# Performance work log

Measured on AMD Instinct MI355X. Metric: run time of the kernel, lower is better.

## Reference

```python
import jax, jax.numpy as jnp
import numpy as np

MARGIN = 0.3

def _cdist(x):
    # pairwise euclidean distances, safe sqrt (zero grad at 0)
    sq = jnp.sum(x * x, axis=1)
    d2 = sq[:, None] + sq[None, :] - 2.0 * (x @ x.T)
    d2 = jnp.maximum(d2, 0.0)
    safe = jnp.where(d2 > 0, d2, 1.0)
    return jnp.where(d2 > 0, jnp.sqrt(safe), 0.0)

def setup_inputs() -> dict:
    key = jax.random.key(0)
    k1, k2 = jax.random.split(key)
    embeddings = jax.random.normal(k1, (4096, 128), dtype=jnp.float32)
    labels = jax.random.randint(k2, (4096,), 0, 256)
    return {"embeddings": embeddings, "labels": labels}

def reference(embeddings, labels):
    B = embeddings.shape[0]
    dist = _cdist(embeddings)                      # [B, B]
    same = labels[:, None] == labels[None, :]      # [B, B]
    eye = jnp.eye(B, dtype=bool)
    pos_mask = same & ~eye
    neg_mask = ~same
    neg_inf = jnp.array(-jnp.inf, dist.dtype)
    pos_inf = jnp.array(jnp.inf, dist.dtype)
    hard_pos = jnp.max(jnp.where(pos_mask, dist, neg_inf), axis=1)  # [B]
    hard_neg = jnp.min(jnp.where(neg_mask, dist, pos_inf), axis=1)  # [B]
    valid = jnp.any(pos_mask, axis=1) & jnp.any(neg_mask, axis=1)
    per_row = jax.nn.relu(hard_pos - hard_neg + MARGIN)
    per_row = jnp.where(valid, per_row, 0.0)
    num_valid = jnp.sum(valid.astype(dist.dtype))
    return jnp.sum(per_row) / jnp.maximum(num_valid, 1.0)
```

## Files before the change

kernel.cpp:

```cpp
#include <hip/hip_runtime.h>
#include <hip/hip_bf16.h>


typedef __attribute__((ext_vector_type(8))) short short8;
typedef __attribute__((ext_vector_type(4))) float f32x4;

#define MARGIN_F 0.3f
#define NEG_BIG -3.4e38f
#define POS_BIG 3.4e38f
#define WAITVM(N) __builtin_amdgcn_s_waitcnt(((N)&15)|((((N)>>4)&3)<<14)|(7<<4)|(15<<8))

__device__ __forceinline__ void gl_lds16(const void* g, void* l) {
    __builtin_amdgcn_global_load_lds(
        (const __attribute__((address_space(1))) void*)g,
        (__attribute__((address_space(3))) void*)l, 16, 0, 0);
}

__device__ inline unsigned short f2bf(float x) {
    union { __hip_bfloat16 h; unsigned short u; } c;
    c.h = __float2bfloat16(x);
    return c.u;
}

__global__ __launch_bounds__(256) void tl_prep(const float* __restrict__ E,
                                               unsigned short* __restrict__ Ebf,
                                               float* __restrict__ sqn,
                                               unsigned* __restrict__ accum) {
    int t = blockIdx.x * 256 + threadIdx.x;
    if (t < 4) accum[t] = 0u;
    int row = t >> 5;
    int kq = (t & 31) * 4;
    float4 v = *(const float4*)&E[(size_t)row * 128 + kq];
    float s = fmaf(v.x, v.x, fmaf(v.y, v.y, fmaf(v.z, v.z, v.w * v.w)));
    ushort4 h4;
    h4.x = f2bf(v.x); h4.y = f2bf(v.y); h4.z = f2bf(v.z); h4.w = f2bf(v.w);
    *(ushort4*)&Ebf[(size_t)row * 128 + kq] = h4;
#pragma unroll
    for (int m = 1; m < 32; m <<= 1) s += __shfl_xor(s, m);
    if ((t & 31) == 0) sqn[row] = s;
}

__global__ __launch_bounds__(256, 2) void tl_phase1(const unsigned short* __restrict__ Ebf,
                                                    const int* __restrict__ labels,
                                                    const float* __restrict__ sqn,
                                                    float* __restrict__ pmp,
                                                    float* __restrict__ pmn) {
    union SM {
        struct { unsigned short A[2][128 * 64]; unsigned short B[2][128 * 64]; } s;
        struct { float mp[128][32]; float mn[128][32];
                 float mpc[128][8]; float mnc[128][8]; } f;
    };
    __shared__ __align__(16) SM sm;

    const int tid = threadIdx.x;
    const int l = tid & 63, w = tid >> 6;
    const int wr = w >> 1, wc = w & 1;
    const int q = l >> 4, r16 = l & 15;

    int t = (int)blockIdx.x;
    int bx = (int)((65.0f - sqrtf((float)(4225 - 8 * t))) * 0.5f);
    while (bx * (65 - bx) / 2 > t) --bx;
    while ((bx + 1) * (64 - bx) / 2 <= t) ++bx;
    const int by = bx + (t - bx * (65 - bx) / 2);
    const int i0 = bx * 128, j0 = by * 128;
    const bool diagblk = (bx == by);

    const unsigned short* gA[4];
    const unsigned short* gB[4];
#pragma unroll
    for (int t2 = 0; t2 < 4; ++t2) {
        int s = w * 256 + t2 * 64 + l;
        int row = s >> 3, ch = (s & 7) ^ (row & 7);
        gA[t2] = Ebf + (size_t)(i0 + row) * 128 + ch * 8;
        gB[t2] = Ebf + (size_t)(j0 + row) * 128 + ch * 8;
    }

    int li[4][4], lj[4];
    float si[4][4], sj[4];
#pragma unroll
    for (int ti = 0; ti < 4; ++ti)
#pragma unroll
        for (int p = 0; p < 4; ++p) {
            int ci = i0 + wr * 64 + ti * 16 + q * 4 + p;
            li[ti][p] = labels[ci];
            si[ti][p] = sqn[ci];
        }
#pragma unroll
    for (int tj = 0; tj < 4; ++tj) {
        int cj = j0 + wc * 64 + tj * 16 + r16;
        lj[tj] = labels[cj];
        sj[tj] = sqn[cj];
    }

#pragma unroll
    for (int t2 = 0; t2 < 4; ++t2) {
        gl_lds16(gA[t2], &sm.s.A[0][w * 2048 + t2 * 512]);
        gl_lds16(gB[t2], &sm.s.B[0][w * 2048 + t2 * 512]);
    }
#pragma unroll
    for (int t2 = 0; t2 < 4; ++t2) {
        gl_lds16(gA[t2] + 64, &sm.s.A[1][w * 2048 + t2 * 512]);
        gl_lds16(gB[t2] + 64, &sm.s.B[1][w * 2048 + t2 * 512]);
    }

    f32x4 acc[4][4];
#pragma unroll
    for (int ti = 0; ti < 4; ++ti)
#pragma unroll
        for (int tj = 0; tj < 4; ++tj) acc[ti][tj] = (f32x4)0.0f;

#pragma unroll
    for (int kc = 0; kc < 2; ++kc) {
        if (kc == 0) WAITVM(8); else WAITVM(0);
        __builtin_amdgcn_s_barrier();
#pragma unroll
        for (int s = 0; s < 2; ++s) {
            short8 af[4], bf[4];
            const int cA = ((s * 4 + q) ^ (r16 & 7)) * 8;
#pragma unroll
            for (int t2 = 0; t2 < 4; ++t2) {
                af[t2] = *(const short8*)&sm.s.A[kc][(wr * 64 + t2 * 16 + r16) * 64 + cA];
                bf[t2] = *(const short8*)&sm.s.B[kc][(wc * 64 + t2 * 16 + r16) * 64 + cA];
            }
#pragma unroll
            for (int ti = 0; ti < 4; ++ti)
#pragma unroll
                for (int tj = 0; tj < 4; ++tj)
                    acc[ti][tj] = __builtin_amdgcn_mfma_f32_16x16x32_bf16(
                        af[ti], bf[tj], acc[ti][tj], 0, 0, 0);
        }
    }

    float mp[4][4], mn[4][4], mpc[4], mnc[4];
#pragma unroll
    for (int ti = 0; ti < 4; ++ti)
#pragma unroll
        for (int p = 0; p < 4; ++p) { mp[ti][p] = NEG_BIG; mn[ti][p] = POS_BIG; }
#pragma unroll
    for (int tj = 0; tj < 4; ++tj) {
        float cp = NEG_BIG, cn = POS_BIG;
#pragma unroll
        for (int ti = 0; ti < 4; ++ti)
#pragma unroll
            for (int p = 0; p < 4; ++p) {
                float g = acc[ti][tj][p];
                float vr = fmaf(-2.0f, g, sj[tj]);
                float vc = fmaf(-2.0f, g, si[ti][p]);
                bool same = (li[ti][p] == lj[tj]);
                bool self = diagblk &&
                    ((wr * 64 + ti * 16 + q * 4 + p) == (wc * 64 + tj * 16 + r16));
                mp[ti][p] = fmaxf(mp[ti][p], (same && !self) ? vr : NEG_BIG);
                mn[ti][p] = fminf(mn[ti][p], same ? POS_BIG : vr);
                cp = fmaxf(cp, (same && !self) ? vc : NEG_BIG);
                cn = fminf(cn, same ? POS_BIG : vc);
            }
        mpc[tj] = cp;
        mnc[tj] = cn;
    }

    __syncthreads();
#pragma unroll
    for (int ti = 0; ti < 4; ++ti)
#pragma unroll
        for (int p = 0; p < 4; ++p) {
            int rloc = wr * 64 + ti * 16 + q * 4 + p;
            sm.f.mp[rloc][wc * 16 + r16] = mp[ti][p];
            sm.f.mn[rloc][wc * 16 + r16] = mn[ti][p];
        }
#pragma unroll
    for (int tj = 0; tj < 4; ++tj) {
        int cloc = wc * 64 + tj * 16 + r16;
        sm.f.mpc[cloc][wr * 4 + q] = mpc[tj];
        sm.f.mnc[cloc][wr * 4 + q] = mnc[tj];
    }
    __syncthreads();
    {
        int row = tid >> 1, hf = tid & 1;
        const float4* P = (const float4*)&sm.f.mp[row][hf * 16];
        const float4* N = (const float4*)&sm.f.mn[row][hf * 16];
        float4 p0 = P[0], p1 = P[1], p2 = P[2], p3 = P[3];
        float4 n0 = N[0], n1 = N[1], n2 = N[2], n3 = N[3];
        float M = fmaxf(fmaxf(fmaxf(p0.x, p0.y), fmaxf(p0.z, p0.w)),
                        fmaxf(fmaxf(p1.x, p1.y), fmaxf(p1.z, p1.w)));
        M = fmaxf(M, fmaxf(fmaxf(fmaxf(p2.x, p2.y), fmaxf(p2.z, p2.w)),
                           fmaxf(fmaxf(p3.x, p3.y), fmaxf(p3.z, p3.w))));
        float m_ = fminf(fminf(fminf(n0.x, n0.y), fminf(n0.z, n0.w)),
                         fminf(fminf(n1.x, n1.y), fminf(n1.z, n1.w)));
        m_ = fminf(m_, fminf(fminf(fminf(n2.x, n2.y), fminf(n2.z, n2.w)),
                             fminf(fminf(n3.x, n3.y), fminf(n3.z, n3.w))));
        M = fmaxf(M, __shfl_xor(M, 1));
        m_ = fminf(m_, __shfl_xor(m_, 1));
        if (hf == 0) {
            pmp[(size_t)by * 4096 + i0 + row] = M;
            pmn[(size_t)by * 4096 + i0 + row] = m_;
        }
    }
    if (!diagblk && tid < 128) {
        const float4* P = (const float4*)&sm.f.mpc[tid][0];
        const float4* N = (const float4*)&sm.f.mnc[tid][0];
        float4 p0 = P[0], p1 = P[1];
        float4 n0 = N[0], n1 = N[1];
        float M = fmaxf(fmaxf(fmaxf(p0.x, p0.y), fmaxf(p0.z, p0.w)),
                        fmaxf(fmaxf(p1.x, p1.y), fmaxf(p1.z, p1.w)));
        float m_ = fminf(fminf(fminf(n0.x, n0.y), fminf(n0.z, n0.w)),
                         fminf(fminf(n1.x, n1.y), fminf(n1.z, n1.w)));
        pmp[(size_t)bx * 4096 + j0 + tid] = M;
        pmn[(size_t)bx * 4096 + j0 + tid] = m_;
    }
}

__global__ __launch_bounds__(256) void tl_phase2(const int* __restrict__ labels,
                                                 const float* __restrict__ pmp,
                                                 const float* __restrict__ pmn,
                                                 const float* __restrict__ sqn,
                                                 float* __restrict__ accum,
                                                 float* __restrict__ out) {
    __shared__ unsigned hist[256];
    __shared__ float sp[4], sv[4];
    int tid = threadIdx.x;
    hist[tid] = 0u;
    __syncthreads();
#pragma unroll
    for (int k = 0; k < 16; ++k) atomicAdd(&hist[labels[k * 256 + tid]], 1u);
    __syncthreads();

    int r = blockIdx.x * 256 + tid;
    float mp = NEG_BIG, mn = POS_BIG;
#pragma unroll
    for (int k = 0; k < 32; ++k) {
        mp = fmaxf(mp, pmp[(size_t)k * 4096 + r]);
        mn = fminf(mn, pmn[(size_t)k * 4096 + r]);
    }
    float si = sqn[r];
    unsigned cnt = hist[labels[r]];
    bool valid = (cnt >= 2u) && (cnt < 4096u);
    float hp = sqrtf(fmaxf(si + mp, 0.0f));
    float hn = sqrtf(fmaxf(si + mn, 0.0f));
    float pr = fmaxf(hp - hn + MARGIN_F, 0.0f);
    float s = valid ? pr : 0.0f;
    float n = valid ? 1.0f : 0.0f;
#pragma unroll
    for (int m = 1; m < 64; m <<= 1) {
        s += __shfl_xor(s, m);
        n += __shfl_xor(n, m);
    }
    if ((tid & 63) == 0) { sp[tid >> 6] = s; sv[tid >> 6] = n; }
    __syncthreads();
    if (tid == 0) {
        float ts = sp[0] + sp[1] + sp[2] + sp[3];
        float tn = sv[0] + sv[1] + sv[2] + sv[3];
        atomicAdd(&accum[0], ts);
        atomicAdd(&accum[1], tn);
        __threadfence();
        unsigned tk = atomicAdd((unsigned*)&accum[2], 1u);
        if (tk == 15u) {
            float a = atomicAdd(&accum[0], 0.0f);
            float b = atomicAdd(&accum[1], 0.0f);
            out[0] = a / fmaxf(b, 1.0f);
        }
    }
}

extern "C" void kernel_launch(void* const* d_in, const int* in_sizes, int n_in,
                              void* d_out, int out_size, void* d_ws, size_t ws_size,
                              hipStream_t stream) {
    const float* E = (const float*)d_in[0];
    const int* labels = (const int*)d_in[1];
    float* out = (float*)d_out;

    char* base = (char*)d_ws;
    unsigned short* Ebf = (unsigned short*)base;
    float* pmp = (float*)(base + (1u << 20));
    float* pmn = (float*)(base + (1u << 20) + (512u << 10));
    float* sqn = (float*)(base + (2u << 20));
    float* accum = (float*)(base + (2u << 20) + (16u << 10));

    tl_prep<<<512, 256, 0, stream>>>(E, Ebf, sqn, (unsigned*)accum);
    tl_phase1<<<528, 256, 0, stream>>>(Ebf, labels, sqn, pmp, pmn);
    tl_phase2<<<16, 256, 0, stream>>>(labels, pmp, pmn, sqn, accum, out);
}
```

Measured before the change: 72.20 us.

## Fuse final reduction into main kernel via atomic min/max and last-block finish

Replaces the per-block-column partial max/min arrays and the separate phase2 kernel with global atomicMax/atomicMin on order-preserving unsigned encodings of the floats. A completion counter lets the last block compute the label histogram, the hinge terms and the final mean, which removes one kernel launch and the 32-way partial reduction pass. In exchange there are atomic contention on 4096 addresses, a single block doing the whole final pass serially, and added fences.

```diff
diff --git a/kernel.cpp b/kernel.cpp
--- a/kernel.cpp
+++ b/kernel.cpp
@@ -22,12 +22,24 @@
     return c.u;
 }
 
+__device__ __forceinline__ unsigned encf(float x) {
+    unsigned u = __float_as_uint(x);
+    return (u >> 31) ? ~u : (u | 0x80000000u);
+}
+__device__ __forceinline__ float decf(unsigned k) {
+    return (k & 0x80000000u) ? __uint_as_float(k ^ 0x80000000u)
+                             : __uint_as_float(~k);
+}
+
 __global__ __launch_bounds__(256) void tl_prep(const float* __restrict__ E,
                                                unsigned short* __restrict__ Ebf,
                                                float* __restrict__ sqn,
-                                               unsigned* __restrict__ accum) {
+                                               unsigned* __restrict__ mpg,
+                                               unsigned* __restrict__ mng,
+                                               unsigned* __restrict__ cnt) {
     int t = blockIdx.x * 256 + threadIdx.x;
-    if (t < 4) accum[t] = 0u;
+    if (t < 4096) { mpg[t] = 0u; mng[t] = 0xFFFFFFFFu; }
+    if (t == 0) cnt[0] = 0u;
     int row = t >> 5;
     int kq = (t & 31) * 4;
     float4 v = *(const float4*)&E[(size_t)row * 128 + kq];
@@ -40,17 +52,22 @@
     if ((t & 31) == 0) sqn[row] = s;
 }
 
-__global__ __launch_bounds__(256, 2) void tl_phase1(const unsigned short* __restrict__ Ebf,
-                                                    const int* __restrict__ labels,
-                                                    const float* __restrict__ sqn,
-                                                    float* __restrict__ pmp,
-                                                    float* __restrict__ pmn) {
+__global__ __launch_bounds__(256, 2) void tl_main(const unsigned short* __restrict__ Ebf,
+                                                  const int* __restrict__ labels,
+                                                  const float* __restrict__ sqn,
+                                                  unsigned* __restrict__ mpg,
+                                                  unsigned* __restrict__ mng,
+                                                  unsigned* __restrict__ cnt,
+                                                  float* __restrict__ out) {
     union SM {
         struct { unsigned short A[2][128 * 64]; unsigned short B[2][128 * 64]; } s;
         struct { float mp[128][32]; float mn[128][32];
                  float mpc[128][8]; float mnc[128][8]; } f;
+        unsigned hist[256];
     };
     __shared__ __align__(16) SM sm;
+    __shared__ int lastblk;
+    __shared__ float sp[4], sv[4];
 
     const int tid = threadIdx.x;
     const int l = tid & 63, w = tid >> 6;
@@ -191,8 +208,8 @@
         M = fmaxf(M, __shfl_xor(M, 1));
         m_ = fminf(m_, __shfl_xor(m_, 1));
         if (hf == 0) {
-            pmp[(size_t)by * 4096 + i0 + row] = M;
-            pmn[(size_t)by * 4096 + i0 + row] = m_;
+            atomicMax(&mpg[i0 + row], encf(M));
+            atomicMin(&mng[i0 + row], encf(m_));
         }
     }
     if (!diagblk && tid < 128) {
@@ -204,41 +221,43 @@
                         fmaxf(fmaxf(p1.x, p1.y), fmaxf(p1.z, p1.w)));
         float m_ = fminf(fminf(fminf(n0.x, n0.y), fminf(n0.z, n0.w)),
                          fminf(fminf(n1.x, n1.y), fminf(n1.z, n1.w)));
-        pmp[(size_t)bx * 4096 + j0 + tid] = M;
-        pmn[(size_t)bx * 4096 + j0 + tid] = m_;
-    }
-}
-
-__global__ __launch_bounds__(256) void tl_phase2(const int* __restrict__ labels,
-                                                 const float* __restrict__ pmp,
-                                                 const float* __restrict__ pmn,
-                                                 const float* __restrict__ sqn,
-                                                 float* __restrict__ accum,
-                                                 float* __restrict__ out) {
-    __shared__ unsigned hist[256];
-    __shared__ float sp[4], sv[4];
-    int tid = threadIdx.x;
-    hist[tid] = 0u;
-    __syncthreads();
-#pragma unroll
-    for (int k = 0; k < 16; ++k) atomicAdd(&hist[labels[k * 256 + tid]], 1u);
-    __syncthreads();
-
-    int r = blockIdx.x * 256 + tid;
-    float mp = NEG_BIG, mn = POS_BIG;
-#pragma unroll
-    for (int k = 0; k < 32; ++k) {
-        mp = fmaxf(mp, pmp[(size_t)k * 4096 + r]);
-        mn = fminf(mn, pmn[(size_t)k * 4096 + r]);
-    }
-    float si = sqn[r];
-    unsigned cnt = hist[labels[r]];
-    bool valid = (cnt >= 2u) && (cnt < 4096u);
-    float hp = sqrtf(fmaxf(si + mp, 0.0f));
-    float hn = sqrtf(fmaxf(si + mn, 0.0f));
-    float pr = fmaxf(hp - hn + MARGIN_F, 0.0f);
-    float s = valid ? pr : 0.0f;
-    float n = valid ? 1.0f : 0.0f;
+        atomicMax(&mpg[j0 + tid], encf(M));
+        atomicMin(&mng[j0 + tid], encf(m_));
+    }
+
+    __syncthreads();
+    if (tid == 0) {
+        __threadfence();
+        lastblk = (atomicAdd(cnt, 1u) == 527u);
+    }
+    __syncthreads();
+    if (!lastblk) return;
+    __threadfence();
+
+    sm.hist[tid] = 0u;
+    __syncthreads();
+    int lab[16];
+#pragma unroll
+    for (int k = 0; k < 16; ++k) {
+        lab[k] = labels[k * 256 + tid];
+        atomicAdd(&sm.hist[lab[k]], 1u);
+    }
+    __syncthreads();
+    float s = 0.0f, n = 0.0f;
+#pragma unroll
+    for (int k = 0; k < 16; ++k) {
+        int r = k * 256 + tid;
+        unsigned kp = __hip_atomic_load(&mpg[r], __ATOMIC_RELAXED, __HIP_MEMORY_SCOPE_AGENT);
+        unsigned kn = __hip_atomic_load(&mng[r], __ATOMIC_RELAXED, __HIP_MEMORY_SCOPE_AGENT);
+        float mpv = decf(kp), mnv = decf(kn);
+        float sir = sqn[r];
+        unsigned c = sm.hist[lab[k]];
+        bool valid = (c >= 2u) && (c < 4096u);
+        float hp = sqrtf(fmaxf(sir + mpv, 0.0f));
+        float hn = sqrtf(fmaxf(sir + mnv, 0.0f));
+        float pr = fmaxf(hp - hn + MARGIN_F, 0.0f);
+        if (valid) { s += pr; n += 1.0f; }
+    }
 #pragma unroll
     for (int m = 1; m < 64; m <<= 1) {
         s += __shfl_xor(s, m);
@@ -249,15 +268,7 @@
     if (tid == 0) {
         float ts = sp[0] + sp[1] + sp[2] + sp[3];
         float tn = sv[0] + sv[1] + sv[2] + sv[3];
-        atomicAdd(&accum[0], ts);
-        atomicAdd(&accum[1], tn);
-        __threadfence();
-        unsigned tk = atomicAdd((unsigned*)&accum[2], 1u);
-        if (tk == 15u) {
-            float a = atomicAdd(&accum[0], 0.0f);
-            float b = atomicAdd(&accum[1], 0.0f);
-            out[0] = a / fmaxf(b, 1.0f);
-        }
+        out[0] = ts / fmaxf(tn, 1.0f);
     }
 }
 
@@ -269,13 +280,12 @@
     float* out = (float*)d_out;
 
     char* base = (char*)d_ws;
-    unsigned short* Ebf = (unsigned short*)base;
-    float* pmp = (float*)(base + (1u << 20));
-    float* pmn = (float*)(base + (1u << 20) + (512u << 10));
-    float* sqn = (float*)(base + (2u << 20));
-    float* accum = (float*)(base + (2u << 20) + (16u << 10));
-
-    tl_prep<<<512, 256, 0, stream>>>(E, Ebf, sqn, (unsigned*)accum);
-    tl_phase1<<<528, 256, 0, stream>>>(Ebf, labels, sqn, pmp, pmn);
-    tl_phase2<<<16, 256, 0, stream>>>(labels, pmp, pmn, sqn, accum, out);
-}
+    unsigned* mpg = (unsigned*)base;
+    unsigned* mng = (unsigned*)(base + (16u << 10));
+    float* sqn = (float*)(base + (32u << 10));
+    unsigned* cnt = (unsigned*)(base + (48u << 10));
+    unsigned short* Ebf = (unsigned short*)(base + (64u << 10));
+
+    tl_prep<<<512, 256, 0, stream>>>(E, Ebf, sqn, mpg, mng, cnt);
+    tl_main<<<528, 256, 0, stream>>>(Ebf, labels, sqn, mpg, mng, cnt, out);
+}
```

Result: slower. 80.02 us (+10.8%).

## Fuse reduction phase into main kernel via ticket counter and shrink LDS

Applied to the files above, without the earlier changes.

Merges the phase-2 row reduction into the tile kernel. Blocks take a ticket when they finish, and the last 16 ticket holders wait on a global counter for all 528 tiles before doing the final per-row min/max and the loss sum. Shared memory is halved by reusing a single K-chunk buffer with a barrier between chunks, and occupancy is raised to 3 blocks per CU. This removes one kernel launch and its gap, but it serialises the two K chunks, which lose their load overlap, and it relies on all blocks being co-resident or scheduled in order so the spin-wait does not deadlock.

```diff
diff --git a/kernel.cpp b/kernel.cpp
--- a/kernel.cpp
+++ b/kernel.cpp
@@ -40,17 +40,23 @@
     if ((t & 31) == 0) sqn[row] = s;
 }
 
-__global__ __launch_bounds__(256, 2) void tl_phase1(const unsigned short* __restrict__ Ebf,
-                                                    const int* __restrict__ labels,
-                                                    const float* __restrict__ sqn,
-                                                    float* __restrict__ pmp,
-                                                    float* __restrict__ pmn) {
+__global__ __launch_bounds__(256, 3) void tl_main(const unsigned short* __restrict__ Ebf,
+                                                  const int* __restrict__ labels,
+                                                  const float* __restrict__ sqn,
+                                                  float* __restrict__ pmp,
+                                                  float* __restrict__ pmn,
+                                                  unsigned* __restrict__ cnt,
+                                                  float* __restrict__ accum,
+                                                  float* __restrict__ out) {
     union SM {
-        struct { unsigned short A[2][128 * 64]; unsigned short B[2][128 * 64]; } s;
+        struct { unsigned short A[128 * 64]; unsigned short B[128 * 64]; } s;
         struct { float mp[128][32]; float mn[128][32];
                  float mpc[128][8]; float mnc[128][8]; } f;
+        unsigned hist[256];
     };
     __shared__ __align__(16) SM sm;
+    __shared__ unsigned myticket;
+    __shared__ float sp[4], sv[4];
 
     const int tid = threadIdx.x;
     const int l = tid & 63, w = tid >> 6;
@@ -75,6 +81,48 @@
         gB[t2] = Ebf + (size_t)(j0 + row) * 128 + ch * 8;
     }
 
+    f32x4 acc[4][4];
+#pragma unroll
+    for (int ti = 0; ti < 4; ++ti)
+#pragma unroll
+        for (int tj = 0; tj < 4; ++tj) acc[ti][tj] = (f32x4)0.0f;
+
+#pragma unroll
+    for (int t2 = 0; t2 < 4; ++t2) {
+        gl_lds16(gA[t2], &sm.s.A[w * 2048 + t2 * 512]);
+        gl_lds16(gB[t2], &sm.s.B[w * 2048 + t2 * 512]);
+    }
+
+#pragma unroll
+    for (int kc = 0; kc < 2; ++kc) {
+        if (kc == 1) {
+            __syncthreads();
+#pragma unroll
+            for (int t2 = 0; t2 < 4; ++t2) {
+                gl_lds16(gA[t2] + 64, &sm.s.A[w * 2048 + t2 * 512]);
+                gl_lds16(gB[t2] + 64, &sm.s.B[w * 2048 + t2 * 512]);
+            }
+        }
+        WAITVM(0);
+        __builtin_amdgcn_s_barrier();
+#pragma unroll
+        for (int s = 0; s < 2; ++s) {
+            short8 af[4], bf[4];
+            const int cA = ((s * 4 + q) ^ (r16 & 7)) * 8;
+#pragma unroll
+            for (int t2 = 0; t2 < 4; ++t2) {
+                af[t2] = *(const short8*)&sm.s.A[(wr * 64 + t2 * 16 + r16) * 64 + cA];
+                bf[t2] = *(const short8*)&sm.s.B[(wc * 64 + t2 * 16 + r16) * 64 + cA];
+            }
+#pragma unroll
+            for (int ti = 0; ti < 4; ++ti)
+#pragma unroll
+                for (int tj = 0; tj < 4; ++tj)
+                    acc[ti][tj] = __builtin_amdgcn_mfma_f32_16x16x32_bf16(
+                        af[ti], bf[tj], acc[ti][tj], 0, 0, 0);
+        }
+    }
+
     int li[4][4], lj[4];
     float si[4][4], sj[4];
 #pragma unroll
@@ -90,45 +138,6 @@
         int cj = j0 + wc * 64 + tj * 16 + r16;
         lj[tj] = labels[cj];
         sj[tj] = sqn[cj];
-    }
-
-#pragma unroll
-    for (int t2 = 0; t2 < 4; ++t2) {
-        gl_lds16(gA[t2], &sm.s.A[0][w * 2048 + t2 * 512]);
-        gl_lds16(gB[t2], &sm.s.B[0][w * 2048 + t2 * 512]);
-    }
-#pragma unroll
-    for (int t2 = 0; t2 < 4; ++t2) {
-        gl_lds16(gA[t2] + 64, &sm.s.A[1][w * 2048 + t2 * 512]);
-        gl_lds16(gB[t2] + 64, &sm.s.B[1][w * 2048 + t2 * 512]);
-    }
-
-    f32x4 acc[4][4];
-#pragma unroll
-    for (int ti = 0; ti < 4; ++ti)
-#pragma unroll
-        for (int tj = 0; tj < 4; ++tj) acc[ti][tj] = (f32x4)0.0f;
-
-#pragma unroll
-    for (int kc = 0; kc < 2; ++kc) {
-        if (kc == 0) WAITVM(8); else WAITVM(0);
-        __builtin_amdgcn_s_barrier();
-#pragma unroll
-        for (int s = 0; s < 2; ++s) {
-            short8 af[4], bf[4];
-            const int cA = ((s * 4 + q) ^ (r16 & 7)) * 8;
-#pragma unroll
-            for (int t2 = 0; t2 < 4; ++t2) {
-                af[t2] = *(const short8*)&sm.s.A[kc][(wr * 64 + t2 * 16 + r16) * 64 + cA];
-                bf[t2] = *(const short8*)&sm.s.B[kc][(wc * 64 + t2 * 16 + r16) * 64 + cA];
-            }
-#pragma unroll
-            for (int ti = 0; ti < 4; ++ti)
-#pragma unroll
-                for (int tj = 0; tj < 4; ++tj)
-                    acc[ti][tj] = __builtin_amdgcn_mfma_f32_16x16x32_bf16(
-                        af[ti], bf[tj], acc[ti][tj], 0, 0, 0);
-        }
     }
 
     float mp[4][4], mn[4][4], mpc[4], mnc[4];
@@ -207,35 +216,45 @@
         pmp[(size_t)bx * 4096 + j0 + tid] = M;
         pmn[(size_t)bx * 4096 + j0 + tid] = m_;
     }
-}
-
-__global__ __launch_bounds__(256) void tl_phase2(const int* __restrict__ labels,
-                                                 const float* __restrict__ pmp,
-                                                 const float* __restrict__ pmn,
-                                                 const float* __restrict__ sqn,
-                                                 float* __restrict__ accum,
-                                                 float* __restrict__ out) {
-    __shared__ unsigned hist[256];
-    __shared__ float sp[4], sv[4];
-    int tid = threadIdx.x;
-    hist[tid] = 0u;
-    __syncthreads();
-#pragma unroll
-    for (int k = 0; k < 16; ++k) atomicAdd(&hist[labels[k * 256 + tid]], 1u);
-    __syncthreads();
-
-    int r = blockIdx.x * 256 + tid;
-    float mp = NEG_BIG, mn = POS_BIG;
+
+    __syncthreads();
+    if (tid == 0)
+        myticket = __hip_atomic_fetch_add(&cnt[0], 1u, __ATOMIC_RELEASE,
+                                          __HIP_MEMORY_SCOPE_AGENT);
+    __syncthreads();
+    unsigned tk = myticket;
+    if (tk < 512u) return;
+
+    if (tid == 0) {
+        while (__hip_atomic_load(&cnt[0], __ATOMIC_ACQUIRE,
+                                 __HIP_MEMORY_SCOPE_AGENT) < 528u)
+            __builtin_amdgcn_s_sleep(8);
+    }
+    __syncthreads();
+    const int slice = (int)(tk - 512u);
+
+    sm.hist[tid] = 0u;
+    __syncthreads();
+#pragma unroll
+    for (int k = 0; k < 16; ++k) atomicAdd(&sm.hist[labels[k * 256 + tid]], 1u);
+    __syncthreads();
+
+    int r = slice * 256 + tid;
+    float fmp = NEG_BIG, fmn = POS_BIG;
 #pragma unroll
     for (int k = 0; k < 32; ++k) {
-        mp = fmaxf(mp, pmp[(size_t)k * 4096 + r]);
-        mn = fminf(mn, pmn[(size_t)k * 4096 + r]);
-    }
-    float si = sqn[r];
-    unsigned cnt = hist[labels[r]];
-    bool valid = (cnt >= 2u) && (cnt < 4096u);
-    float hp = sqrtf(fmaxf(si + mp, 0.0f));
-    float hn = sqrtf(fmaxf(si + mn, 0.0f));
+        float vp = __hip_atomic_load(&pmp[(size_t)k * 4096 + r], __ATOMIC_RELAXED,
+                                     __HIP_MEMORY_SCOPE_AGENT);
+        float vn = __hip_atomic_load(&pmn[(size_t)k * 4096 + r], __ATOMIC_RELAXED,
+                                     __HIP_MEMORY_SCOPE_AGENT);
+        fmp = fmaxf(fmp, vp);
+        fmn = fminf(fmn, vn);
+    }
+    float sir = sqn[r];
+    unsigned c = sm.hist[labels[r]];
+    bool valid = (c >= 2u) && (c < 4096u);
+    float hp = sqrtf(fmaxf(sir + fmp, 0.0f));
+    float hn = sqrtf(fmaxf(sir + fmn, 0.0f));
     float pr = fmaxf(hp - hn + MARGIN_F, 0.0f);
     float s = valid ? pr : 0.0f;
     float n = valid ? 1.0f : 0.0f;
@@ -249,13 +268,13 @@
     if (tid == 0) {
         float ts = sp[0] + sp[1] + sp[2] + sp[3];
         float tn = sv[0] + sv[1] + sv[2] + sv[3];
-        atomicAdd(&accum[0], ts);
-        atomicAdd(&accum[1], tn);
-        __threadfence();
-        unsigned tk = atomicAdd((unsigned*)&accum[2], 1u);
-        if (tk == 15u) {
-            float a = atomicAdd(&accum[0], 0.0f);
-            float b = atomicAdd(&accum[1], 0.0f);
+        __hip_atomic_fetch_add(&accum[0], ts, __ATOMIC_RELAXED, __HIP_MEMORY_SCOPE_AGENT);
+        __hip_atomic_fetch_add(&accum[1], tn, __ATOMIC_RELAXED, __HIP_MEMORY_SCOPE_AGENT);
+        unsigned tk2 = __hip_atomic_fetch_add(&cnt[1], 1u, __ATOMIC_ACQ_REL,
+                                              __HIP_MEMORY_SCOPE_AGENT);
+        if (tk2 == 15u) {
+            float a = __hip_atomic_load(&accum[0], __ATOMIC_RELAXED, __HIP_MEMORY_SCOPE_AGENT);
+            float b = __hip_atomic_load(&accum[1], __ATOMIC_RELAXED, __HIP_MEMORY_SCOPE_AGENT);
             out[0] = a / fmaxf(b, 1.0f);
         }
     }
@@ -274,8 +293,8 @@
     float* pmn = (float*)(base + (1u << 20) + (512u << 10));
     float* sqn = (float*)(base + (2u << 20));
     float* accum = (float*)(base + (2u << 20) + (16u << 10));
+    unsigned* cnt = (unsigned*)(accum + 2);
 
     tl_prep<<<512, 256, 0, stream>>>(E, Ebf, sqn, (unsigned*)accum);
-    tl_phase1<<<528, 256, 0, stream>>>(Ebf, labels, sqn, pmp, pmn);
-    tl_phase2<<<16, 256, 0, stream>>>(labels, pmp, pmn, sqn, accum, out);
-}
+    tl_main<<<528, 256, 0, stream>>>(Ebf, labels, sqn, pmp, pmn, cnt, accum, out);
+}
```

New measurement: 79.61 us. 1.1x slower.

## Fold diagonal tiles into off-diagonal blocks to shrink phase1 grid

Applied to the files above, without the earlier changes.

The 32 diagonal 128x128 tiles are no longer separate blocks. Each one is computed as a second MFMA tile inside a host off-diagonal block: the superdiagonal block, plus block (0,31) for the last diagonal, reusing the LDS data it already holds. This cuts the grid from 528 to 496 blocks, which is intended to reduce tail or wave imbalance, and it drops the self-mask check from the main path. The host blocks do twice the MFMA work and carry an extra accumulator set that raises register pressure. Label and sqn loads for rows are also vectorised to int4/float4.

```diff
diff --git a/kernel.cpp b/kernel.cpp
--- a/kernel.cpp
+++ b/kernel.cpp
@@ -58,12 +58,17 @@
     const int q = l >> 4, r16 = l & 15;
 
     int t = (int)blockIdx.x;
-    int bx = (int)((65.0f - sqrtf((float)(4225 - 8 * t))) * 0.5f);
-    while (bx * (65 - bx) / 2 > t) --bx;
-    while ((bx + 1) * (64 - bx) / 2 <= t) ++bx;
-    const int by = bx + (t - bx * (65 - bx) / 2);
+    int bx = (int)((63.0f - sqrtf((float)(3969 - 8 * t))) * 0.5f);
+    while (bx * (63 - bx) / 2 > t) --bx;
+    while ((bx + 1) * (62 - bx) / 2 <= t) ++bx;
+    const int by = bx + 1 + (t - bx * (63 - bx) / 2);
     const int i0 = bx * 128, j0 = by * 128;
-    const bool diagblk = (bx == by);
+
+    const bool hostA = (by == bx + 1);
+    const bool hostB = (bx == 0) && (by == 31);
+    const bool hasdiag = hostA || hostB;
+    const int dbase = hostA ? i0 : j0;
+    const int dslot = hostA ? bx : by;
 
     const unsigned short* gA[4];
     const unsigned short* gB[4];
@@ -78,13 +83,13 @@
     int li[4][4], lj[4];
     float si[4][4], sj[4];
 #pragma unroll
-    for (int ti = 0; ti < 4; ++ti)
-#pragma unroll
-        for (int p = 0; p < 4; ++p) {
-            int ci = i0 + wr * 64 + ti * 16 + q * 4 + p;
-            li[ti][p] = labels[ci];
-            si[ti][p] = sqn[ci];
-        }
+    for (int ti = 0; ti < 4; ++ti) {
+        int cb = i0 + wr * 64 + ti * 16 + q * 4;
+        int4 lv = *(const int4*)&labels[cb];
+        float4 sv = *(const float4*)&sqn[cb];
+        li[ti][0] = lv.x; li[ti][1] = lv.y; li[ti][2] = lv.z; li[ti][3] = lv.w;
+        si[ti][0] = sv.x; si[ti][1] = sv.y; si[ti][2] = sv.z; si[ti][3] = sv.w;
+    }
 #pragma unroll
     for (int tj = 0; tj < 4; ++tj) {
         int cj = j0 + wc * 64 + tj * 16 + r16;
@@ -103,16 +108,23 @@
         gl_lds16(gB[t2] + 64, &sm.s.B[1][w * 2048 + t2 * 512]);
     }
 
-    f32x4 acc[4][4];
+    f32x4 acc[4][4], accd[4][4];
 #pragma unroll
     for (int ti = 0; ti < 4; ++ti)
 #pragma unroll
         for (int tj = 0; tj < 4; ++tj) acc[ti][tj] = (f32x4)0.0f;
+    if (hasdiag) {
+#pragma unroll
+        for (int ti = 0; ti < 4; ++ti)
+#pragma unroll
+            for (int tj = 0; tj < 4; ++tj) accd[ti][tj] = (f32x4)0.0f;
+    }
 
 #pragma unroll
     for (int kc = 0; kc < 2; ++kc) {
         if (kc == 0) WAITVM(8); else WAITVM(0);
         __builtin_amdgcn_s_barrier();
+        const unsigned short* Dk = hostA ? &sm.s.A[kc][0] : &sm.s.B[kc][0];
 #pragma unroll
         for (int s = 0; s < 2; ++s) {
             short8 af[4], bf[4];
@@ -128,6 +140,20 @@
                 for (int tj = 0; tj < 4; ++tj)
                     acc[ti][tj] = __builtin_amdgcn_mfma_f32_16x16x32_bf16(
                         af[ti], bf[tj], acc[ti][tj], 0, 0, 0);
+            if (hasdiag) {
+                short8 dA[4], dB[4];
+#pragma unroll
+                for (int t2 = 0; t2 < 4; ++t2) {
+                    dA[t2] = *(const short8*)&Dk[(wr * 64 + t2 * 16 + r16) * 64 + cA];
+                    dB[t2] = *(const short8*)&Dk[(wc * 64 + t2 * 16 + r16) * 64 + cA];
+                }
+#pragma unroll
+                for (int ti = 0; ti < 4; ++ti)
+#pragma unroll
+                    for (int tj = 0; tj < 4; ++tj)
+                        accd[ti][tj] = __builtin_amdgcn_mfma_f32_16x16x32_bf16(
+                            dA[ti], dB[tj], accd[ti][tj], 0, 0, 0);
+            }
         }
     }
 
@@ -147,11 +173,9 @@
                 float vr = fmaf(-2.0f, g, sj[tj]);
                 float vc = fmaf(-2.0f, g, si[ti][p]);
                 bool same = (li[ti][p] == lj[tj]);
-                bool self = diagblk &&
-                    ((wr * 64 + ti * 16 + q * 4 + p) == (wc * 64 + tj * 16 + r16));
-                mp[ti][p] = fmaxf(mp[ti][p], (same && !self) ? vr : NEG_BIG);
+                mp[ti][p] = fmaxf(mp[ti][p], same ? vr : NEG_BIG);
                 mn[ti][p] = fminf(mn[ti][p], same ? POS_BIG : vr);
-                cp = fmaxf(cp, (same && !self) ? vc : NEG_BIG);
+                cp = fmaxf(cp, same ? vc : NEG_BIG);
                 cn = fminf(cn, same ? POS_BIG : vc);
             }
         mpc[tj] = cp;
@@ -195,7 +219,7 @@
             pmn[(size_t)by * 4096 + i0 + row] = m_;
         }
     }
-    if (!diagblk && tid < 128) {
+    if (tid < 128) {
         const float4* P = (const float4*)&sm.f.mpc[tid][0];
         const float4* N = (const float4*)&sm.f.mnc[tid][0];
         float4 p0 = P[0], p1 = P[1];
@@ -206,6 +230,72 @@
                          fminf(fminf(n1.x, n1.y), fminf(n1.z, n1.w)));
         pmp[(size_t)bx * 4096 + j0 + tid] = M;
         pmn[(size_t)bx * 4096 + j0 + tid] = m_;
+    }
+
+    if (hasdiag) {
+        int ldr[4][4], ldc[4];
+        float sdc[4];
+#pragma unroll
+        for (int ti = 0; ti < 4; ++ti) {
+            int cb = dbase + wr * 64 + ti * 16 + q * 4;
+            int4 lv = *(const int4*)&labels[cb];
+            ldr[ti][0] = lv.x; ldr[ti][1] = lv.y; ldr[ti][2] = lv.z; ldr[ti][3] = lv.w;
+        }
+#pragma unroll
+        for (int tj = 0; tj < 4; ++tj) {
+            int cd = dbase + wc * 64 + tj * 16 + r16;
+            ldc[tj] = labels[cd];
+            sdc[tj] = sqn[cd];
+        }
+        float mpd[4][4], mnd[4][4];
+#pragma unroll
+        for (int ti = 0; ti < 4; ++ti)
+#pragma unroll
+            for (int p = 0; p < 4; ++p) { mpd[ti][p] = NEG_BIG; mnd[ti][p] = POS_BIG; }
+#pragma unroll
+        for (int tj = 0; tj < 4; ++tj) {
+#pragma unroll
+            for (int ti = 0; ti < 4; ++ti)
+#pragma unroll
+                for (int p = 0; p < 4; ++p) {
+                    float g = accd[ti][tj][p];
+                    float v = fmaf(-2.0f, g, sdc[tj]);
+                    bool same = (ldr[ti][p] == ldc[tj]);
+                    bool self = (wr * 64 + ti * 16 + q * 4 + p) ==
+                                (wc * 64 + tj * 16 + r16);
+                    mpd[ti][p] = fmaxf(mpd[ti][p], (same && !self) ? v : NEG_BIG);
+                    mnd[ti][p] = fminf(mnd[ti][p], same ? POS_BIG : v);
+                }
+        }
+        __syncthreads();
+#pragma unroll
+        for (int ti = 0; ti < 4; ++ti)
+#pragma unroll
+            for (int p = 0; p < 4; ++p) {
+                int rloc = wr * 64 + ti * 16 + q * 4 + p;
+                sm.f.mp[rloc][wc * 16 + r16] = mpd[ti][p];
+                sm.f.mn[rloc][wc * 16 + r16] = mnd[ti][p];
+            }
+        __syncthreads();
+        int row = tid >> 1, hf = tid & 1;
+        const float4* P = (const float4*)&sm.f.mp[row][hf * 16];
+        const float4* N = (const float4*)&sm.f.mn[row][hf * 16];
+        float4 p0 = P[0], p1 = P[1], p2 = P[2], p3 = P[3];
+        float4 n0 = N[0], n1 = N[1], n2 = N[2], n3 = N[3];
+        float M = fmaxf(fmaxf(fmaxf(p0.x, p0.y), fmaxf(p0.z, p0.w)),
+                        fmaxf(fmaxf(p1.x, p1.y), fmaxf(p1.z, p1.w)));
+        M = fmaxf(M, fmaxf(fmaxf(fmaxf(p2.x, p2.y), fmaxf(p2.z, p2.w)),
+                           fmaxf(fmaxf(p3.x, p3.y), fmaxf(p3.z, p3.w))));
+        float m_ = fminf(fminf(fminf(n0.x, n0.y), fminf(n0.z, n0.w)),
+                         fminf(fminf(n1.x, n1.y), fminf(n1.z, n1.w)));
+        m_ = fminf(m_, fminf(fminf(fminf(n2.x, n2.y), fminf(n2.z, n2.w)),
+                             fminf(fminf(n3.x, n3.y), fminf(n3.z, n3.w))));
+        M = fmaxf(M, __shfl_xor(M, 1));
+        m_ = fminf(m_, __shfl_xor(m_, 1));
+        if (hf == 0) {
+            pmp[(size_t)dslot * 4096 + dbase + row] = M;
+            pmn[(size_t)dslot * 4096 + dbase + row] = m_;
+        }
     }
 }
 
@@ -276,6 +366,6 @@
     float* accum = (float*)(base + (2u << 20) + (16u << 10));
 
     tl_prep<<<512, 256, 0, stream>>>(E, Ebf, sqn, (unsigned*)accum);
-    tl_phase1<<<528, 256, 0, stream>>>(Ebf, labels, sqn, pmp, pmn);
+    tl_phase1<<<496, 256, 0, stream>>>(Ebf, labels, sqn, pmp, pmn);
     tl_phase2<<<16, 256, 0, stream>>>(labels, pmp, pmn, sqn, accum, out);
 }
```

Measured after the change: 72.47 us. Within noise of the previous version (+0.4%).
